# Kernel optimization log

Hardware: AMD Instinct MI355X
Metric: run time of the kernel (lower is better)

The kernel has to match this reference:

```python
import math
import jax, jax.numpy as jnp
import numpy as np

B, M, N, D, H = 64, 5, 1000, 128, 8
KS = D // H
TANH_CLIP = 10.0

def setup_inputs() -> dict:
    key = jax.random.key(0)
    ks = jax.random.split(key, 12)
    mask = jax.random.randint(ks[8], (B, M, N), 0, 2).astype(bool)
    mask = mask.at[:, 0, 0].set(True)  # guarantee at least one feasible action per batch row
    return {
        'node_embeddings': jax.random.normal(ks[0], (B, N, D), jnp.float32),
        'fixed_context': jax.random.normal(ks[1], (B, 1, D), jnp.float32),
        'prev_node_embeddings': jax.random.normal(ks[2], (B, M, D), jnp.float32),
        'node_dynamic_features': jax.random.normal(ks[3], (B, M, N, 8), jnp.float32),
        'vehicle_dynamic_features': jax.random.normal(ks[4], (B, M, 3), jnp.float32),
        'glimpse_V_static': jax.random.normal(ks[5], (H, B, 1, N, KS), jnp.float32),
        'glimpse_K_static': jax.random.normal(ks[6], (H, B, 1, N, KS), jnp.float32),
        'logit_K_static': jax.random.normal(ks[7], (B, 1, N, D), jnp.float32),
        'feasibility_mask': mask,
        'W_pcv': jax.random.normal(ks[9], (D, D + 3), jnp.float32) * 0.05,
        'W_pns': jax.random.normal(ks[10], (3 * D, 8), jnp.float32) * 0.05,
        'po_weight': jax.random.normal(ks[11], (D, D), jnp.float32) * 0.05,
    }

def reference(node_embeddings, fixed_context, prev_node_embeddings,
              node_dynamic_features, vehicle_dynamic_features,
              glimpse_V_static, glimpse_K_static, logit_K_static,
              feasibility_mask, W_pcv, W_pns, po_weight):
    # current vehicle state projection: [B,M,D]
    cvs = jnp.concatenate([prev_node_embeddings, vehicle_dynamic_features], axis=-1)
    proj_cvs = cvs @ W_pcv.T
    # dynamic node embeddings: [B,M,N,3D] -> three [B,M,N,D] chunks
    nde = node_dynamic_features @ W_pns.T
    gVd, gKd, lKd = jnp.split(nde, 3, axis=-1)
    # make heads: [B,M,N,D] -> [H,B,M,N,KS]
    def mh(x):
        return x.reshape(B, M, N, H, KS).transpose(3, 0, 1, 2, 4)
    glimpse_V = glimpse_V_static + mh(gVd)  # [H,B,M,N,KS]
    glimpse_K = glimpse_K_static + mh(gKd)
    logit_K = logit_K_static + lKd          # [B,M,N,D]
    query = fixed_context + proj_cvs        # [B,M,D]
    Q = query.reshape(B, M, H, KS).transpose(2, 0, 1, 3)  # [H,B,M,KS]
    mask_log = jnp.log(feasibility_mask.astype(jnp.float32))  # [B,M,N]
    compat = jnp.einsum('hbmk,hbmnk->hbmn', Q, glimpse_K) / math.sqrt(KS)
    compat = compat + mask_log[None]
    # softmax over joint vehicle*node axis
    attn = jax.nn.softmax(compat.reshape(H, B, M * N), axis=-1).reshape(H, B, M, N)
    heads = jnp.einsum('hbmn,hbmnk->hbmk', attn, glimpse_V)  # [H,B,M,KS]
    concat = heads.transpose(1, 2, 0, 3).reshape(B, M, D)
    final_Q = concat @ po_weight.T          # [B,M,D]
    logits = jnp.einsum('bmd,bmnd->bmn', final_Q, logit_K) / math.sqrt(D)
    logits = jnp.tanh(logits) * TANH_CLIP + mask_log
    probs = jax.nn.softmax(logits.reshape(B, M * N), axis=-1)
    return probs
```

## Files before the change

kernel.cpp:

```cpp
#include <hip/hip_runtime.h>
#include <cstddef>

#define BB 64
#define MM 5
#define NN 1000
#define DD 128
#define HH 8
#define KSZ 16
#define NCH 4
#define CH2 250
#define NC3 8
#define CH3 125
#define INV_SQRT_D 0.08838834764831845f

__device__ __forceinline__ float tanh_fast(float x) {
  float e = __expf(2.f * x);
  return 1.f - 2.f / (e + 1.f);
}

__global__ __launch_bounds__(256) void k1_query(
    const float* __restrict__ fc, const float* __restrict__ pne,
    const float* __restrict__ vdf, const float* __restrict__ wpcv,
    const float* __restrict__ wpns, float* __restrict__ q_ws,
    float* __restrict__ qw_ws)
{
  const int bm = blockIdx.x;
  const int b = bm / MM;
  const int m = bm % MM;
  const int t = threadIdx.x;
  const int k = t & 15, gid = t >> 4;
  __shared__ float qsh[DD];

  float cvr[9];
  const float* pner = pne + (size_t)bm * DD;
#pragma unroll
  for (int jp = 0; jp < 8; ++jp) cvr[jp] = pner[k + 16 * jp];
  cvr[8] = (k < 3) ? vdf[bm * 3 + k] : 0.f;

#pragma unroll 2
  for (int dd = 0; dd < 8; ++dd) {
    const int d = gid + 16 * dd;
    const float* wrow = wpcv + d * 131;
    float p = 0.f;
#pragma unroll
    for (int jp = 0; jp < 8; ++jp) p = fmaf(cvr[jp], wrow[k + 16 * jp], p);
    if (k < 3) p = fmaf(cvr[8], wrow[128 + k], p);
    p += __shfl_xor(p, 1); p += __shfl_xor(p, 2);
    p += __shfl_xor(p, 4); p += __shfl_xor(p, 8);
    if (k == 0) {
      const float q = 0.25f * (p + fc[b * DD + d]);
      qsh[d] = q;
      q_ws[(size_t)bm * DD + d] = q;
    }
  }
  __syncthreads();
  if (t < 64) {
    const int h = t >> 3, f = t & 7;
    float acc = 0.f;
#pragma unroll
    for (int kk = 0; kk < KSZ; ++kk)
      acc = fmaf(qsh[h * KSZ + kk], wpns[(DD + h * KSZ + kk) * 8 + f], acc);
    qw_ws[(b * HH + h) * 40 + m * 8 + f] = acc;
  }
}

__global__ __launch_bounds__(256) void k2_attn(
    const float* __restrict__ ndf, const float* __restrict__ gV,
    const float* __restrict__ gK, const int* __restrict__ mask,
    const float* __restrict__ q_ws, const float* __restrict__ qw_ws,
    float* __restrict__ part)
{
  const int blk = blockIdx.x;
  const int c = blk & 3;
  const int h = (blk >> 2) & 7;
  const int b = blk >> 5;
  const int t = threadIdx.x;
  const int k = t & 7, gid = t >> 3;
  const int n0 = c * CH2;

  float2 qr[MM];
  float qwr[MM];
#pragma unroll
  for (int m = 0; m < MM; ++m) {
    qr[m] = *(const float2*)(q_ws + (size_t)(b * MM + m) * DD + h * KSZ + 2 * k);
    qwr[m] = qw_ws[(b * HH + h) * 40 + m * 8 + k];
  }
  float2 hacc[MM] = {};
  float afv[MM] = {};
  float lsum = 0.f;

  const float* kbase = gK + ((size_t)(h * BB + b) * NN + n0) * KSZ;
  const float* vbase = gV + ((size_t)(h * BB + b) * NN + n0) * KSZ;
  const float* nbase = ndf + (size_t)(b * MM) * NN * 8;
  const int* mbase = mask + (size_t)(b * MM) * NN;

  auto body = [&](int nl) {
    const float2 kv = *(const float2*)(kbase + nl * KSZ + 2 * k);
    const float2 vv = *(const float2*)(vbase + nl * KSZ + 2 * k);
    float ndv[MM]; int mk[MM];
#pragma unroll
    for (int m = 0; m < MM; ++m) {
      const size_t roff = (size_t)m * NN + n0 + nl;
      ndv[m] = nbase[roff * 8 + k];
      mk[m] = mbase[roff];
    }
#pragma unroll
    for (int m = 0; m < MM; ++m) {
      float p = kv.x * qr[m].x + kv.y * qr[m].y + ndv[m] * qwr[m];
      p += __shfl_xor(p, 1); p += __shfl_xor(p, 2); p += __shfl_xor(p, 4);
      const float e = mk[m] ? __expf(p) : 0.f;
      hacc[m].x = fmaf(e, vv.x, hacc[m].x);
      hacc[m].y = fmaf(e, vv.y, hacc[m].y);
      afv[m] = fmaf(e, ndv[m], afv[m]);
      lsum += e;
    }
  };

#pragma unroll 2
  for (int i = 0; i < 7; ++i) body(gid + 32 * i);
  if (gid + 224 < CH2) body(gid + 224);

#pragma unroll
  for (int m = 0; m < MM; ++m) {
    hacc[m].x += __shfl_xor(hacc[m].x, 8);
    hacc[m].x += __shfl_xor(hacc[m].x, 16);
    hacc[m].x += __shfl_xor(hacc[m].x, 32);
    hacc[m].y += __shfl_xor(hacc[m].y, 8);
    hacc[m].y += __shfl_xor(hacc[m].y, 16);
    hacc[m].y += __shfl_xor(hacc[m].y, 32);
    afv[m] += __shfl_xor(afv[m], 8);
    afv[m] += __shfl_xor(afv[m], 16);
    afv[m] += __shfl_xor(afv[m], 32);
  }
  lsum += __shfl_xor(lsum, 8);
  lsum += __shfl_xor(lsum, 16);
  lsum += __shfl_xor(lsum, 32);

  __shared__ float redh[4][MM][KSZ];
  __shared__ float redaf[4][MM][8];
  __shared__ float reds[4];
  const int w = t >> 6;
  if ((t & 63) < 8) {
    const int kk = t & 7;
#pragma unroll
    for (int m = 0; m < MM; ++m) {
      redh[w][m][2 * kk] = hacc[m].x;
      redh[w][m][2 * kk + 1] = hacc[m].y;
      redaf[w][m][kk] = afv[m];
    }
  }
  if ((t & 63) == 0) reds[w] = lsum;
  __syncthreads();
  float* P = part + (size_t)blk * 128;
  if (t < 80) {
    const int m = t >> 4, kk = t & 15;
    P[t] = redh[0][m][kk] + redh[1][m][kk] + redh[2][m][kk] + redh[3][m][kk];
  } else if (t < 120) {
    const int r = t - 80, m = r >> 3, f = r & 7;
    P[80 + r] = redaf[0][m][f] + redaf[1][m][f] + redaf[2][m][f] + redaf[3][m][f];
  } else if (t == 120) {
    P[120] = reds[0] + reds[1] + reds[2] + reds[3];
  }
}

__global__ __launch_bounds__(256) void k2b_combine(
    const float* __restrict__ part, const float* __restrict__ wpns,
    const float* __restrict__ po, float* __restrict__ fq_ws,
    float* __restrict__ fw_ws)
{
  const int b = blockIdx.x;
  const int t = threadIdx.x;
  __shared__ float pos[DD][129];
  __shared__ float rgs[HH];
  __shared__ float afs[HH][MM][8];
  __shared__ float cs[MM][DD];
  __shared__ float fqs[MM][DD];

  for (int i = t; i < DD * DD / 4; i += 256) {
    const float4 v = ((const float4*)po)[i];
    const int r = (i * 4) >> 7, cc = (i * 4) & 127;
    pos[r][cc] = v.x; pos[r][cc + 1] = v.y; pos[r][cc + 2] = v.z; pos[r][cc + 3] = v.w;
  }
  const float* pb = part + (size_t)b * 32 * 128;
  if (t < HH) {
    float s = 0.f;
#pragma unroll
    for (int c = 0; c < NCH; ++c) s += pb[(t * 4 + c) * 128 + 120];
    rgs[t] = 1.f / s;
  }
  for (int idx = t; idx < HH * MM * 8; idx += 256) {
    const int h = idx / 40, r = idx % 40;
    float a = 0.f;
#pragma unroll
    for (int c = 0; c < NCH; ++c) a += pb[(h * 4 + c) * 128 + 80 + r];
    afs[h][r >> 3][r & 7] = a;
  }
  __syncthreads();
  for (int idx = t; idx < MM * DD; idx += 256) {
    const int m = idx >> 7, d = idx & 127, h = d >> 4;
    float a = 0.f;
#pragma unroll
    for (int c = 0; c < NCH; ++c) a += pb[(h * 4 + c) * 128 + m * 16 + (d & 15)];
    float cf = 0.f;
#pragma unroll
    for (int f = 0; f < 8; ++f) cf = fmaf(wpns[d * 8 + f], afs[h][m][f], cf);
    cs[m][d] = (a + cf) * rgs[h];
  }
  __syncthreads();
  for (int idx = t; idx < MM * DD; idx += 256) {
    const int m = idx >> 7, d = idx & 127;
    float acc = 0.f;
#pragma unroll 8
    for (int j = 0; j < DD; ++j) acc = fmaf(cs[m][j], pos[d][j], acc);
    acc *= INV_SQRT_D;
    fqs[m][d] = acc;
    fq_ws[(size_t)b * (MM * DD) + idx] = acc;
  }
  __syncthreads();
  if (t < MM * 8) {
    const int m = t >> 3, f = t & 7;
    float acc = 0.f;
#pragma unroll 16
    for (int d = 0; d < DD; ++d) acc = fmaf(fqs[m][d], wpns[(2 * DD + d) * 8 + f], acc);
    fw_ws[b * 40 + t] = acc;
  }
}

__global__ __launch_bounds__(512) void k3_logits(
    const float* __restrict__ ndf, const float* __restrict__ lK,
    const int* __restrict__ mask, const float* __restrict__ fq_ws,
    const float* __restrict__ fw_ws, float* __restrict__ out,
    float* __restrict__ stats)
{
  const int b = blockIdx.x >> 3;
  const int c = blockIdx.x & 7;
  const int t = threadIdx.x;
  const int k = t & 15, gid = t >> 4;
  const int n0 = c * CH3;

  float2 fqr[MM][4];
  float fwr[MM];
#pragma unroll
  for (int m = 0; m < MM; ++m) {
#pragma unroll
    for (int jp = 0; jp < 4; ++jp)
      fqr[m][jp] = *(const float2*)(fq_ws + (size_t)(b * MM + m) * DD + 32 * jp + 2 * k);
    fwr[m] = fw_ws[b * 40 + m * 8 + (k & 7)];
  }
  float lsum = 0.f;

#pragma unroll
  for (int i = 0; i < 4; ++i) {
    const int nl = gid + 32 * i;
    const bool valid = (nl < CH3);
    const int n = n0 + (valid ? nl : 0);
    const float* lkr = lK + ((size_t)b * NN + n) * DD;
    const float2 lk0 = *(const float2*)(lkr + 2 * k);
    const float2 lk1 = *(const float2*)(lkr + 32 + 2 * k);
    const float2 lk2 = *(const float2*)(lkr + 64 + 2 * k);
    const float2 lk3 = *(const float2*)(lkr + 96 + 2 * k);
    float ndv[MM]; int mk[MM];
#pragma unroll
    for (int m = 0; m < MM; ++m) {
      const size_t roff = (size_t)(b * MM + m) * NN + n;
      ndv[m] = ndf[roff * 8 + (k & 7)];
      mk[m] = mask[roff];
    }
#pragma unroll
    for (int m = 0; m < MM; ++m) {
      float p = lk0.x * fqr[m][0].x + lk0.y * fqr[m][0].y
              + lk1.x * fqr[m][1].x + lk1.y * fqr[m][1].y
              + lk2.x * fqr[m][2].x + lk2.y * fqr[m][2].y
              + lk3.x * fqr[m][3].x + lk3.y * fqr[m][3].y;
      p += (k < 8) ? ndv[m] * fwr[m] : 0.f;
      p += __shfl_xor(p, 1); p += __shfl_xor(p, 2);
      p += __shfl_xor(p, 4); p += __shfl_xor(p, 8);
      const float e = mk[m] ? __expf(tanh_fast(p) * 10.f) : 0.f;
      if (valid) {
        lsum += e;
        if (k == 0) out[(size_t)(b * MM + m) * NN + n] = e;
      }
    }
  }
  lsum += __shfl_xor(lsum, 16);
  lsum += __shfl_xor(lsum, 32);
  __shared__ float wred[8];
  if ((t & 63) == 0) wred[t >> 6] = lsum;
  __syncthreads();
  if (t == 0) {
    float s = 0.f;
#pragma unroll
    for (int w = 0; w < 8; ++w) s += wred[w];
    stats[b * NC3 + c] = s;
  }
}

__global__ __launch_bounds__(256) void k4_probs(
    const float* __restrict__ stats, float* __restrict__ out)
{
  const int bm = blockIdx.x;
  const int b = bm / MM;
  const int t = threadIdx.x;
  float s = 0.f;
#pragma unroll
  for (int c = 0; c < NC3; ++c) s += stats[b * NC3 + c];
  const float scale = 1.f / s;
  if (t < 250) {
    float4* p = (float4*)(out + (size_t)bm * NN);
    float4 v = p[t];
    v.x *= scale; v.y *= scale; v.z *= scale; v.w *= scale;
    p[t] = v;
  }
}

extern "C" void kernel_launch(void* const* d_in, const int* in_sizes, int n_in,
                              void* d_out, int out_size, void* d_ws, size_t ws_size,
                              hipStream_t stream) {
  const float* fc   = (const float*)d_in[1];
  const float* pne  = (const float*)d_in[2];
  const float* ndf  = (const float*)d_in[3];
  const float* vdf  = (const float*)d_in[4];
  const float* gV   = (const float*)d_in[5];
  const float* gK   = (const float*)d_in[6];
  const float* lK   = (const float*)d_in[7];
  const int*   mask = (const int*)d_in[8];
  const float* wpcv = (const float*)d_in[9];
  const float* wpns = (const float*)d_in[10];
  const float* po   = (const float*)d_in[11];

  float* q_ws  = (float*)d_ws;
  float* qw_ws = q_ws + BB * MM * DD;
  float* part  = qw_ws + BB * HH * MM * 8;
  float* fq_ws = part + (size_t)BB * HH * NCH * 128;
  float* fw_ws = fq_ws + BB * MM * DD;
  float* stats = fw_ws + BB * 40;
  float* out   = (float*)d_out;

  k1_query<<<BB * MM, 256, 0, stream>>>(fc, pne, vdf, wpcv, wpns, q_ws, qw_ws);
  k2_attn<<<BB * HH * NCH, 256, 0, stream>>>(ndf, gV, gK, mask, q_ws, qw_ws, part);
  k2b_combine<<<BB, 256, 0, stream>>>(part, wpns, po, fq_ws, fw_ws);
  k3_logits<<<BB * NC3, 512, 0, stream>>>(ndf, lK, mask, fq_ws, fw_ws, out, stats);
  k4_probs<<<BB * MM, 256, 0, stream>>>(stats, out);
}
```

Baseline: 62.25 us.

## Pack feasibility mask into per-node bitmask and widen attention/logit loads

Adds extra blocks to the query kernel that pack the five per-vehicle mask ints for each node into one bitmask word, which the attention and logits kernels then read instead of five separate ints. The attention kernel goes from 8 to 4 lanes per node so it can use float4 K/V loads and float2 dynamic-feature loads, with four fully unrolled iterations. The logits kernel switches to float4 loads of logit_K in a contiguous per-lane layout. This cuts mask traffic and the number of memory instructions. In exchange the attention kernel gets more registers per thread and fewer lanes share each reduction, and k3 k4 still read the mask launch order via bitmask workspace.

Measured after the change: 58.85 us. 1.06x faster.

```diff
diff --git a/kernel.cpp b/kernel.cpp
--- a/kernel.cpp
+++ b/kernel.cpp
@@ -21,13 +21,24 @@
 __global__ __launch_bounds__(256) void k1_query(
     const float* __restrict__ fc, const float* __restrict__ pne,
     const float* __restrict__ vdf, const float* __restrict__ wpcv,
-    const float* __restrict__ wpns, float* __restrict__ q_ws,
-    float* __restrict__ qw_ws)
-{
+    const float* __restrict__ wpns, const int* __restrict__ mask,
+    float* __restrict__ q_ws, float* __restrict__ qw_ws,
+    unsigned int* __restrict__ pmask)
+{
+  const int t = threadIdx.x;
+  if (blockIdx.x >= BB * MM) {
+    const int b = blockIdx.x - BB * MM;
+    const int* mb = mask + (size_t)(b * MM) * NN;
+    for (int n = t; n < NN; n += 256) {
+      unsigned int pm = 0;
+#pragma unroll
+      for (int m = 0; m < MM; ++m) pm |= (mb[m * NN + n] != 0 ? 1u : 0u) << m;
+      pmask[b * NN + n] = pm;
+    }
+    return;
+  }
   const int bm = blockIdx.x;
   const int b = bm / MM;
-  const int m = bm % MM;
-  const int t = threadIdx.x;
   const int k = t & 15, gid = t >> 4;
   __shared__ float qsh[DD];
 
@@ -60,13 +71,13 @@
 #pragma unroll
     for (int kk = 0; kk < KSZ; ++kk)
       acc = fmaf(qsh[h * KSZ + kk], wpns[(DD + h * KSZ + kk) * 8 + f], acc);
-    qw_ws[(b * HH + h) * 40 + m * 8 + f] = acc;
+    qw_ws[(b * HH + h) * 40 + (bm % MM) * 8 + f] = acc;
   }
 }
 
 __global__ __launch_bounds__(256) void k2_attn(
     const float* __restrict__ ndf, const float* __restrict__ gV,
-    const float* __restrict__ gK, const int* __restrict__ mask,
+    const float* __restrict__ gK, const unsigned int* __restrict__ pmask,
     const float* __restrict__ q_ws, const float* __restrict__ qw_ws,
     float* __restrict__ part)
 {
@@ -75,78 +86,82 @@
   const int h = (blk >> 2) & 7;
   const int b = blk >> 5;
   const int t = threadIdx.x;
-  const int k = t & 7, gid = t >> 3;
+  const int k = t & 3, gid = t >> 2;
   const int n0 = c * CH2;
 
-  float2 qr[MM];
-  float qwr[MM];
+  float4 qr[MM];
+  float2 qwr[MM];
 #pragma unroll
   for (int m = 0; m < MM; ++m) {
-    qr[m] = *(const float2*)(q_ws + (size_t)(b * MM + m) * DD + h * KSZ + 2 * k);
-    qwr[m] = qw_ws[(b * HH + h) * 40 + m * 8 + k];
-  }
-  float2 hacc[MM] = {};
-  float afv[MM] = {};
+    qr[m] = *(const float4*)(q_ws + (size_t)(b * MM + m) * DD + h * KSZ + 4 * k);
+    qwr[m] = *(const float2*)(qw_ws + (b * HH + h) * 40 + m * 8 + 2 * k);
+  }
+  float4 hacc[MM] = {};
+  float2 afv[MM] = {};
   float lsum = 0.f;
 
   const float* kbase = gK + ((size_t)(h * BB + b) * NN + n0) * KSZ;
   const float* vbase = gV + ((size_t)(h * BB + b) * NN + n0) * KSZ;
-  const float* nbase = ndf + (size_t)(b * MM) * NN * 8;
-  const int* mbase = mask + (size_t)(b * MM) * NN;
-
-  auto body = [&](int nl) {
-    const float2 kv = *(const float2*)(kbase + nl * KSZ + 2 * k);
-    const float2 vv = *(const float2*)(vbase + nl * KSZ + 2 * k);
-    float ndv[MM]; int mk[MM];
+  const float* nbase = ndf + ((size_t)(b * MM) * NN + n0) * 8;
+  const unsigned int* pmb = pmask + b * NN + n0;
+
+#pragma unroll
+  for (int i = 0; i < 4; ++i) {
+    const int nl = gid + 64 * i;
+    const bool valid = (nl < CH2);
+    const int nc = valid ? nl : 0;
+    const unsigned int pm = valid ? pmb[nc] : 0u;
+    const float4 kv = *(const float4*)(kbase + nc * KSZ + 4 * k);
+    const float4 vv = *(const float4*)(vbase + nc * KSZ + 4 * k);
+    float2 ndv[MM];
+#pragma unroll
+    for (int m = 0; m < MM; ++m)
+      ndv[m] = *(const float2*)(nbase + ((size_t)m * NN + nc) * 8 + 2 * k);
 #pragma unroll
     for (int m = 0; m < MM; ++m) {
-      const size_t roff = (size_t)m * NN + n0 + nl;
-      ndv[m] = nbase[roff * 8 + k];
-      mk[m] = mbase[roff];
-    }
-#pragma unroll
-    for (int m = 0; m < MM; ++m) {
-      float p = kv.x * qr[m].x + kv.y * qr[m].y + ndv[m] * qwr[m];
-      p += __shfl_xor(p, 1); p += __shfl_xor(p, 2); p += __shfl_xor(p, 4);
-      const float e = mk[m] ? __expf(p) : 0.f;
+      float p = kv.x * qr[m].x + kv.y * qr[m].y + kv.z * qr[m].z + kv.w * qr[m].w
+              + ndv[m].x * qwr[m].x + ndv[m].y * qwr[m].y;
+      p += __shfl_xor(p, 1); p += __shfl_xor(p, 2);
+      const float e = ((pm >> m) & 1u) ? __expf(p) : 0.f;
       hacc[m].x = fmaf(e, vv.x, hacc[m].x);
       hacc[m].y = fmaf(e, vv.y, hacc[m].y);
-      afv[m] = fmaf(e, ndv[m], afv[m]);
+      hacc[m].z = fmaf(e, vv.z, hacc[m].z);
+      hacc[m].w = fmaf(e, vv.w, hacc[m].w);
+      afv[m].x = fmaf(e, ndv[m].x, afv[m].x);
+      afv[m].y = fmaf(e, ndv[m].y, afv[m].y);
       lsum += e;
     }
-  };
-
-#pragma unroll 2
-  for (int i = 0; i < 7; ++i) body(gid + 32 * i);
-  if (gid + 224 < CH2) body(gid + 224);
+  }
 
 #pragma unroll
   for (int m = 0; m < MM; ++m) {
-    hacc[m].x += __shfl_xor(hacc[m].x, 8);
-    hacc[m].x += __shfl_xor(hacc[m].x, 16);
-    hacc[m].x += __shfl_xor(hacc[m].x, 32);
-    hacc[m].y += __shfl_xor(hacc[m].y, 8);
-    hacc[m].y += __shfl_xor(hacc[m].y, 16);
-    hacc[m].y += __shfl_xor(hacc[m].y, 32);
-    afv[m] += __shfl_xor(afv[m], 8);
-    afv[m] += __shfl_xor(afv[m], 16);
-    afv[m] += __shfl_xor(afv[m], 32);
-  }
-  lsum += __shfl_xor(lsum, 8);
-  lsum += __shfl_xor(lsum, 16);
-  lsum += __shfl_xor(lsum, 32);
+#pragma unroll
+    for (int off = 4; off <= 32; off <<= 1) {
+      hacc[m].x += __shfl_xor(hacc[m].x, off);
+      hacc[m].y += __shfl_xor(hacc[m].y, off);
+      hacc[m].z += __shfl_xor(hacc[m].z, off);
+      hacc[m].w += __shfl_xor(hacc[m].w, off);
+      afv[m].x += __shfl_xor(afv[m].x, off);
+      afv[m].y += __shfl_xor(afv[m].y, off);
+    }
+  }
+#pragma unroll
+  for (int off = 4; off <= 32; off <<= 1) lsum += __shfl_xor(lsum, off);
 
   __shared__ float redh[4][MM][KSZ];
   __shared__ float redaf[4][MM][8];
   __shared__ float reds[4];
   const int w = t >> 6;
-  if ((t & 63) < 8) {
-    const int kk = t & 7;
+  if ((t & 63) < 4) {
+    const int kk = t & 3;
 #pragma unroll
     for (int m = 0; m < MM; ++m) {
-      redh[w][m][2 * kk] = hacc[m].x;
-      redh[w][m][2 * kk + 1] = hacc[m].y;
-      redaf[w][m][kk] = afv[m];
+      redh[w][m][4 * kk + 0] = hacc[m].x;
+      redh[w][m][4 * kk + 1] = hacc[m].y;
+      redh[w][m][4 * kk + 2] = hacc[m].z;
+      redh[w][m][4 * kk + 3] = hacc[m].w;
+      redaf[w][m][2 * kk + 0] = afv[m].x;
+      redaf[w][m][2 * kk + 1] = afv[m].y;
     }
   }
   if ((t & 63) == 0) reds[w] = lsum;
@@ -228,7 +243,7 @@
 
 __global__ __launch_bounds__(512) void k3_logits(
     const float* __restrict__ ndf, const float* __restrict__ lK,
-    const int* __restrict__ mask, const float* __restrict__ fq_ws,
+    const unsigned int* __restrict__ pmask, const float* __restrict__ fq_ws,
     const float* __restrict__ fw_ws, float* __restrict__ out,
     float* __restrict__ stats)
 {
@@ -238,13 +253,12 @@
   const int k = t & 15, gid = t >> 4;
   const int n0 = c * CH3;
 
-  float2 fqr[MM][4];
+  float4 fqr[MM][2];
   float fwr[MM];
 #pragma unroll
   for (int m = 0; m < MM; ++m) {
-#pragma unroll
-    for (int jp = 0; jp < 4; ++jp)
-      fqr[m][jp] = *(const float2*)(fq_ws + (size_t)(b * MM + m) * DD + 32 * jp + 2 * k);
+    fqr[m][0] = *(const float4*)(fq_ws + (size_t)(b * MM + m) * DD + 8 * k);
+    fqr[m][1] = *(const float4*)(fq_ws + (size_t)(b * MM + m) * DD + 8 * k + 4);
     fwr[m] = fw_ws[b * 40 + m * 8 + (k & 7)];
   }
   float lsum = 0.f;
@@ -254,28 +268,24 @@
     const int nl = gid + 32 * i;
     const bool valid = (nl < CH3);
     const int n = n0 + (valid ? nl : 0);
+    const unsigned int pm = valid ? pmask[b * NN + n] : 0u;
     const float* lkr = lK + ((size_t)b * NN + n) * DD;
-    const float2 lk0 = *(const float2*)(lkr + 2 * k);
-    const float2 lk1 = *(const float2*)(lkr + 32 + 2 * k);
-    const float2 lk2 = *(const float2*)(lkr + 64 + 2 * k);
-    const float2 lk3 = *(const float2*)(lkr + 96 + 2 * k);
-    float ndv[MM]; int mk[MM];
+    const float4 l0 = *(const float4*)(lkr + 8 * k);
+    const float4 l1 = *(const float4*)(lkr + 8 * k + 4);
+    float ndv[MM];
+#pragma unroll
+    for (int m = 0; m < MM; ++m)
+      ndv[m] = (k < 8) ? ndf[((size_t)(b * MM + m) * NN + n) * 8 + k] : 0.f;
 #pragma unroll
     for (int m = 0; m < MM; ++m) {
-      const size_t roff = (size_t)(b * MM + m) * NN + n;
-      ndv[m] = ndf[roff * 8 + (k & 7)];
-      mk[m] = mask[roff];
-    }
-#pragma unroll
-    for (int m = 0; m < MM; ++m) {
-      float p = lk0.x * fqr[m][0].x + lk0.y * fqr[m][0].y
-              + lk1.x * fqr[m][1].x + lk1.y * fqr[m][1].y
-              + lk2.x * fqr[m][2].x + lk2.y * fqr[m][2].y
-              + lk3.x * fqr[m][3].x + lk3.y * fqr[m][3].y;
-      p += (k < 8) ? ndv[m] * fwr[m] : 0.f;
+      float p = l0.x * fqr[m][0].x + l0.y * fqr[m][0].y
+              + l0.z * fqr[m][0].z + l0.w * fqr[m][0].w
+              + l1.x * fqr[m][1].x + l1.y * fqr[m][1].y
+              + l1.z * fqr[m][1].z + l1.w * fqr[m][1].w
+              + ndv[m] * fwr[m];
       p += __shfl_xor(p, 1); p += __shfl_xor(p, 2);
       p += __shfl_xor(p, 4); p += __shfl_xor(p, 8);
-      const float e = mk[m] ? __expf(tanh_fast(p) * 10.f) : 0.f;
+      const float e = ((pm >> m) & 1u) ? __expf(tanh_fast(p) * 10.f) : 0.f;
       if (valid) {
         lsum += e;
         if (k == 0) out[(size_t)(b * MM + m) * NN + n] = e;
@@ -334,11 +344,13 @@
   float* fq_ws = part + (size_t)BB * HH * NCH * 128;
   float* fw_ws = fq_ws + BB * MM * DD;
   float* stats = fw_ws + BB * 40;
+  unsigned int* pmask = (unsigned int*)(stats + BB * NC3);
   float* out   = (float*)d_out;
 
-  k1_query<<<BB * MM, 256, 0, stream>>>(fc, pne, vdf, wpcv, wpns, q_ws, qw_ws);
-  k2_attn<<<BB * HH * NCH, 256, 0, stream>>>(ndf, gV, gK, mask, q_ws, qw_ws, part);
+  k1_query<<<BB * MM + BB, 256, 0, stream>>>(fc, pne, vdf, wpcv, wpns, mask,
+                                             q_ws, qw_ws, pmask);
+  k2_attn<<<BB * HH * NCH, 256, 0, stream>>>(ndf, gV, gK, pmask, q_ws, qw_ws, part);
   k2b_combine<<<BB, 256, 0, stream>>>(part, wpns, po, fq_ws, fw_ws);
-  k3_logits<<<BB * NC3, 512, 0, stream>>>(ndf, lK, mask, fq_ws, fw_ws, out, stats);
+  k3_logits<<<BB * NC3, 512, 0, stream>>>(ndf, lK, pmask, fq_ws, fw_ws, out, stats);
   k4_probs<<<BB * MM, 256, 0, stream>>>(stats, out);
 }
```
